# Optimization experiments

Hardware: AMD Instinct MI355X
Metric: run time of the kernel (lower is better)

The kernel has to match this reference:

```python
import jax, jax.numpy as jnp
import numpy as np

LOSS_CUTOFF = 100000.0
EPS = 1e-08

B, S, A = 512, 512, 200


def setup_inputs() -> dict:
    key = jax.random.key(0)
    k1, k2, k3, k4 = jax.random.split(key, 4)
    logits = jax.random.normal(k1, (B, S, A), dtype=jnp.float32)
    actions = jax.random.randint(k2, (B, S), 0, A, dtype=jnp.int64)
    rewards = jax.random.uniform(k3, (B, S), dtype=jnp.float32)
    terminals = jax.random.uniform(k4, (B, S), dtype=jnp.float32)
    return {"logits": logits, "actions": actions, "rewards": rewards, "terminals": terminals}


def reference(logits, actions, rewards, terminals):
    # log_p: [B, S, A], masked by (1 - terminals)
    log_p = jax.nn.log_softmax(logits, axis=2) * (1.0 - terminals)[:, :, None]
    # gather per-timestep action log-prob: [B, S] -> total_logp: [B]
    action_logp = jnp.take_along_axis(log_p, actions[:, :, None], axis=2)[..., 0]
    total_logp = -jnp.sum(action_logp, axis=1)  # [B]
    total_rewards = jnp.sum(rewards, axis=1)    # [B]
    # 'mean' branch: masked mean over total_logp < loss_cutoff
    prod = total_logp * total_rewards
    mask = total_logp < LOSS_CUTOFF
    cnt = jnp.sum(mask.astype(prod.dtype))
    rewardloss_mean = jnp.sum(jnp.where(mask, prod, 0.0)) / cnt
    mean_loss = rewardloss_mean / (jnp.mean(jnp.abs(total_rewards)) + EPS)
    return mean_loss
```

## Files before the change

### kernel.cpp

```cpp
#include <hip/hip_runtime.h>
#include <hip/hip_bf16.h>
#include <math.h>


#define BDIM 512
#define SDIM 512
#define ADIM 200
#define ROWS_PER_WAVE 8
#define WAVES_PER_BLOCK 4
#define ROWS_PER_ITER (ROWS_PER_WAVE * WAVES_PER_BLOCK)
#define ITERS 4
#define ROWS_PER_BLOCK (ROWS_PER_ITER * ITERS)
#define NBLOCKS ((BDIM * SDIM) / ROWS_PER_BLOCK)

__device__ __forceinline__ float dpp_reduce_add(float x) {
    int t;
    t = __builtin_amdgcn_update_dpp(0, __float_as_int(x), 0x111, 0xf, 0xf, true); x += __int_as_float(t);
    t = __builtin_amdgcn_update_dpp(0, __float_as_int(x), 0x112, 0xf, 0xf, true); x += __int_as_float(t);
    t = __builtin_amdgcn_update_dpp(0, __float_as_int(x), 0x114, 0xf, 0xf, true); x += __int_as_float(t);
    t = __builtin_amdgcn_update_dpp(0, __float_as_int(x), 0x118, 0xf, 0xf, true); x += __int_as_float(t);
    t = __builtin_amdgcn_update_dpp(0, __float_as_int(x), 0x142, 0xa, 0xf, true); x += __int_as_float(t);
    t = __builtin_amdgcn_update_dpp(0, __float_as_int(x), 0x143, 0xc, 0xf, true); x += __int_as_float(t);
    return x;
}

__global__ __launch_bounds__(256, 4) void pg_row_kernel(
    const float* __restrict__ logits,
    const int*   __restrict__ actions,
    const float* __restrict__ rewards,
    const float* __restrict__ terminals,
    float* __restrict__ ws_logp,
    float* __restrict__ ws_rew)
{
    const int lane = threadIdx.x & 63;
    const int wave = threadIdx.x >> 6;
    const int block_row0 = blockIdx.x * ROWS_PER_BLOCK;
    const int b = block_row0 >> 9;

    const int  cl = (lane < 50) ? lane : 49;

    float acc_logp = 0.0f, acc_rew = 0.0f;

    for (int it = 0; it < ITERS; ++it) {
        const int row0 = block_row0 + it * ROWS_PER_ITER + wave * ROWS_PER_WAVE;

        int a[ROWS_PER_WAVE];
        #pragma unroll
        for (int i = 0; i < ROWS_PER_WAVE; ++i) a[i] = actions[row0 + i];

        float4 v[ROWS_PER_WAVE];
        #pragma unroll
        for (int i = 0; i < ROWS_PER_WAVE; ++i)
            v[i] = ((const float4*)(logits + (size_t)(row0 + i) * ADIM))[cl];

        float xa[ROWS_PER_WAVE], tm[ROWS_PER_WAVE], rw[ROWS_PER_WAVE];
        #pragma unroll
        for (int i = 0; i < ROWS_PER_WAVE; ++i) {
            xa[i] = logits[(size_t)(row0 + i) * ADIM + a[i]];
            tm[i] = terminals[row0 + i];
            rw[i] = rewards[row0 + i];
        }

        #pragma unroll
        for (int i = 0; i < ROWS_PER_WAVE; ++i) {
            float s = __expf(v[i].x) + __expf(v[i].y) +
                      __expf(v[i].z) + __expf(v[i].w);
            s = (lane < 50) ? s : 0.0f;
            const float tot  = dpp_reduce_add(s);
            const float etot = __int_as_float(
                __builtin_amdgcn_readlane(__float_as_int(tot), 63));
            acc_logp += (xa[i] - __logf(etot)) * (1.0f - tm[i]);
            acc_rew  += rw[i];
        }
    }

    __shared__ float s_logp[WAVES_PER_BLOCK], s_rew[WAVES_PER_BLOCK];
    if (lane == 0) { s_logp[wave] = acc_logp; s_rew[wave] = acc_rew; }
    __syncthreads();
    if (threadIdx.x == 0) {
        float tl = 0.0f, tr = 0.0f;
        #pragma unroll
        for (int w = 0; w < WAVES_PER_BLOCK; ++w) { tl += s_logp[w]; tr += s_rew[w]; }
        atomicAdd(&ws_logp[b], tl);
        atomicAdd(&ws_rew[b],  tr);
    }
}

__global__ __launch_bounds__(512) void pg_final_kernel(
    const float* __restrict__ ws_logp,
    const float* __restrict__ ws_rew,
    float* __restrict__ out)
{
    const int tid  = threadIdx.x;
    const int lane = tid & 63;
    const int wave = tid >> 6;

    const float total_logp = -ws_logp[tid];
    const float total_rew  =  ws_rew[tid];

    float mp   = (total_logp < 100000.0f) ? total_logp * total_rew : 0.0f;
    float cnt  = (total_logp < 100000.0f) ? 1.0f : 0.0f;
    float arew = fabsf(total_rew);

    #pragma unroll
    for (int off = 32; off >= 1; off >>= 1) {
        mp   += __shfl_down(mp,   off);
        cnt  += __shfl_down(cnt,  off);
        arew += __shfl_down(arew, off);
    }

    __shared__ float s_mp[8], s_cnt[8], s_ab[8];
    if (lane == 0) { s_mp[wave] = mp; s_cnt[wave] = cnt; s_ab[wave] = arew; }
    __syncthreads();
    if (tid == 0) {
        float smp = 0.0f, scnt = 0.0f, sab = 0.0f;
        #pragma unroll
        for (int i = 0; i < 8; ++i) { smp += s_mp[i]; scnt += s_cnt[i]; sab += s_ab[i]; }
        const float rewardloss_mean = smp / scnt;
        out[0] = rewardloss_mean / (sab / (float)BDIM + 1e-8f);
    }
}

extern "C" void kernel_launch(void* const* d_in, const int* in_sizes, int n_in,
                              void* d_out, int out_size, void* d_ws, size_t ws_size,
                              hipStream_t stream) {
    const float* logits    = (const float*)d_in[0];
    const int*   actions   = (const int*)  d_in[1];
    const float* rewards   = (const float*)d_in[2];
    const float* terminals = (const float*)d_in[3];

    float* ws_logp = (float*)d_ws;
    float* ws_rew  = ws_logp + BDIM;

    hipMemsetAsync(d_ws, 0, 2 * BDIM * sizeof(float), stream);

    pg_row_kernel<<<NBLOCKS, 256, 0, stream>>>(
        logits, actions, rewards, terminals, ws_logp, ws_rew);

    pg_final_kernel<<<1, 512, 0, stream>>>(ws_logp, ws_rew, (float*)d_out);
}
```

Measured before the change: 292.1 us.

## Gather action logit via shuffle, vectorize side loads, nontemporal loads, one pass per block

Each block now handles 32 rows in a single pass instead of four iterations, so there are four times as many blocks and four times as many atomics per batch row. Actions, terminals and rewards are read as int4/float4 vectors. The per-row gather of the action's logit is replaced by selecting the value from registers and moving it with a wave shuffle, which removes a dependent scattered global load. Logit loads use nontemporal hints to avoid cache pollution on this streaming read.

```diff
diff --git a/kernel.cpp b/kernel.cpp
--- a/kernel.cpp
+++ b/kernel.cpp
@@ -8,10 +8,10 @@
 #define ADIM 200
 #define ROWS_PER_WAVE 8
 #define WAVES_PER_BLOCK 4
-#define ROWS_PER_ITER (ROWS_PER_WAVE * WAVES_PER_BLOCK)
-#define ITERS 4
-#define ROWS_PER_BLOCK (ROWS_PER_ITER * ITERS)
+#define ROWS_PER_BLOCK (ROWS_PER_WAVE * WAVES_PER_BLOCK)
 #define NBLOCKS ((BDIM * SDIM) / ROWS_PER_BLOCK)
+
+typedef float nf4 __attribute__((ext_vector_type(4)));
 
 __device__ __forceinline__ float dpp_reduce_add(float x) {
     int t;
@@ -34,44 +34,45 @@
 {
     const int lane = threadIdx.x & 63;
     const int wave = threadIdx.x >> 6;
-    const int block_row0 = blockIdx.x * ROWS_PER_BLOCK;
-    const int b = block_row0 >> 9;
+    const int row0 = blockIdx.x * ROWS_PER_BLOCK + wave * ROWS_PER_WAVE;
+    const int b    = blockIdx.x >> 4;
 
-    const int  cl = (lane < 50) ? lane : 49;
+    const int cl = (lane < 50) ? lane : 49;
+
+    const int4*   ap = (const int4*)  (actions   + row0);
+    const float4* tp = (const float4*)(terminals + row0);
+    const float4* rp = (const float4*)(rewards   + row0);
+    const int4   a03 = ap[0], a47 = ap[1];
+    const float4 t03 = tp[0], t47 = tp[1];
+    const float4 r03 = rp[0], r47 = rp[1];
+    const int   a[ROWS_PER_WAVE]  = {a03.x, a03.y, a03.z, a03.w, a47.x, a47.y, a47.z, a47.w};
+    const float tm[ROWS_PER_WAVE] = {t03.x, t03.y, t03.z, t03.w, t47.x, t47.y, t47.z, t47.w};
+    const float rw[ROWS_PER_WAVE] = {r03.x, r03.y, r03.z, r03.w, r47.x, r47.y, r47.z, r47.w};
+
+    nf4 v[ROWS_PER_WAVE];
+    #pragma unroll
+    for (int i = 0; i < ROWS_PER_WAVE; ++i) {
+        const nf4* rowp = (const nf4*)(logits + (size_t)(row0 + i) * ADIM);
+        v[i] = __builtin_nontemporal_load(rowp + cl);
+    }
 
     float acc_logp = 0.0f, acc_rew = 0.0f;
+    #pragma unroll
+    for (int i = 0; i < ROWS_PER_WAVE; ++i) {
+        const int   sub  = a[i] & 3;
+        const float cand = (sub == 0) ? v[i].x : (sub == 1) ? v[i].y
+                         : (sub == 2) ? v[i].z : v[i].w;
+        const float xa   = __shfl(cand, a[i] >> 2);
 
-    for (int it = 0; it < ITERS; ++it) {
-        const int row0 = block_row0 + it * ROWS_PER_ITER + wave * ROWS_PER_WAVE;
+        float s = __expf(v[i].x) + __expf(v[i].y) +
+                  __expf(v[i].z) + __expf(v[i].w);
+        s = (lane < 50) ? s : 0.0f;
+        const float tot  = dpp_reduce_add(s);
+        const float etot = __int_as_float(
+            __builtin_amdgcn_readlane(__float_as_int(tot), 63));
 
-        int a[ROWS_PER_WAVE];
-        #pragma unroll
-        for (int i = 0; i < ROWS_PER_WAVE; ++i) a[i] = actions[row0 + i];
-
-        float4 v[ROWS_PER_WAVE];
-        #pragma unroll
-        for (int i = 0; i < ROWS_PER_WAVE; ++i)
-            v[i] = ((const float4*)(logits + (size_t)(row0 + i) * ADIM))[cl];
-
-        float xa[ROWS_PER_WAVE], tm[ROWS_PER_WAVE], rw[ROWS_PER_WAVE];
-        #pragma unroll
-        for (int i = 0; i < ROWS_PER_WAVE; ++i) {
-            xa[i] = logits[(size_t)(row0 + i) * ADIM + a[i]];
-            tm[i] = terminals[row0 + i];
-            rw[i] = rewards[row0 + i];
-        }
-
-        #pragma unroll
-        for (int i = 0; i < ROWS_PER_WAVE; ++i) {
-            float s = __expf(v[i].x) + __expf(v[i].y) +
-                      __expf(v[i].z) + __expf(v[i].w);
-            s = (lane < 50) ? s : 0.0f;
-            const float tot  = dpp_reduce_add(s);
-            const float etot = __int_as_float(
-                __builtin_amdgcn_readlane(__float_as_int(tot), 63));
-            acc_logp += (xa[i] - __logf(etot)) * (1.0f - tm[i]);
-            acc_rew  += rw[i];
-        }
+        acc_logp += (xa - __logf(etot)) * (1.0f - tm[i]);
+        acc_rew  += rw[i];
     }
 
     __shared__ float s_logp[WAVES_PER_BLOCK], s_rew[WAVES_PER_BLOCK];
@@ -132,7 +133,7 @@
     float* ws_logp = (float*)d_ws;
     float* ws_rew  = ws_logp + BDIM;
 
-    hipMemsetAsync(d_ws, 0, 2 * BDIM * sizeof(float), stream);
+    (void)hipMemsetAsync(d_ws, 0, 2 * BDIM * sizeof(float), stream);
 
     pg_row_kernel<<<NBLOCKS, 256, 0, stream>>>(
         logits, actions, rewards, terminals, ws_logp, ws_rew);
```

Result: faster. 277.2 us (-5.1%).
